# Performance work log

Hardware: AMD Instinct MI355X
Metric: run time of the kernel (lower is better)

## Reference

```python
import jax, jax.numpy as jnp
import numpy as np

XBOUND = (-30.0, 30.0, 0.25)
YBOUND = (-15.0, 15.0, 0.25)
ZBOUND = (-1.0, 1.0, 0.5)
EPS = 1e-9


def _heights():
    n = int((ZBOUND[1] - ZBOUND[0]) // ZBOUND[2]) + 1
    return [ZBOUND[0] + i * ZBOUND[2] for i in range(n)]


def _bev_planes():
    # matches construct_plane_grid: linspace endpoints included, meshgrid(y, x) 'ij'
    num_x = int((XBOUND[1] - XBOUND[0]) / XBOUND[2])
    num_y = int((YBOUND[1] - YBOUND[0]) / YBOUND[2])
    x = jnp.linspace(XBOUND[0], XBOUND[1], num_x, dtype=jnp.float32)
    y = jnp.linspace(YBOUND[0], YBOUND[1], num_y, dtype=jnp.float32)
    yy, xx = jnp.meshgrid(y, x, indexing='ij')
    planes = [jnp.stack([xx, yy, jnp.full_like(xx, h)], axis=-1) for h in _heights()]
    return jnp.stack(planes)  # (nlvl, bH, bW, 3)


def _bilinear_grid_sample(im, grid):
    # faithful port of the manual pad+floor+gather grid_sample (align_corners=False)
    n, c, h, w = im.shape
    gh, gw = grid.shape[1], grid.shape[2]
    x = ((grid[..., 0] + 1) * w - 1) / 2
    y = ((grid[..., 1] + 1) * h - 1) / 2
    x = x.reshape(n, -1)
    y = y.reshape(n, -1)
    x0 = jnp.floor(x)
    y0 = jnp.floor(y)
    wa = ((x0 + 1 - x) * (y0 + 1 - y))[:, None, :]
    wb = ((x0 + 1 - x) * (y - y0))[:, None, :]
    wc = ((x - x0) * (y0 + 1 - y))[:, None, :]
    wd = ((x - x0) * (y - y0))[:, None, :]
    pw, ph = w + 2, h + 2
    # clip in float first to avoid int32 overflow; out-of-range lands on zero padding either way
    x0f = jnp.clip(x0, -2.0, w + 2.0)
    y0f = jnp.clip(y0, -2.0, h + 2.0)
    x0i = jnp.clip(x0f.astype(jnp.int32) + 1, 0, pw - 1)
    x1i = jnp.clip(x0f.astype(jnp.int32) + 2, 0, pw - 1)
    y0i = jnp.clip(y0f.astype(jnp.int32) + 1, 0, ph - 1)
    y1i = jnp.clip(y0f.astype(jnp.int32) + 2, 0, ph - 1)
    im_flat = jnp.pad(im, ((0, 0), (0, 0), (1, 1), (1, 1))).reshape(n, c, -1)

    def gather(xi, yi):
        return jnp.take_along_axis(im_flat, (xi + yi * pw)[:, None, :], axis=2)

    out = (gather(x0i, y0i) * wa + gather(x0i, y1i) * wb
           + gather(x1i, y0i) * wc + gather(x1i, y1i) * wd)
    return out.reshape(n, c, gh, gw)


def _campos(pts, ego2cam, img_h, img_w):
    # pts: (B, q, 3); ego2cam: (B, ncam, 4, 4)
    B, q, _ = pts.shape
    ncam = ego2cam.shape[1]
    pts_h = jnp.concatenate([pts, jnp.ones_like(pts[..., :1])], axis=-1)  # (B,q,4)
    cam = jnp.einsum('bnij,bqj->bnqi', ego2cam, pts_h)  # (B,ncam,q,4)
    z = cam[..., 2:3]
    mask = z > EPS
    xy = cam[..., 0:2] / z + EPS
    px = xy[..., 0:1] / img_w
    py = xy[..., 1:2] / img_h
    p = (jnp.concatenate([px, py], axis=-1) - 0.5) * 2
    mask = (mask & (p[..., 0:1] > -1.0) & (p[..., 0:1] < 1.0)
            & (p[..., 1:2] > -1.0) & (p[..., 1:2] < 1.0))
    return p.reshape(B * ncam, q, 2), mask.reshape(B, ncam, q)


def reference(cam_feat, ego2cam, conv_w, conv_b, img_h, img_w):
    B, ncam = ego2cam.shape[0], ego2cam.shape[1]
    C = cam_feat.shape[1]
    planes = _bev_planes().astype(cam_feat.dtype)  # (nlvl,bH,bW,3)
    nlvl, bH, bW, _ = planes.shape
    pts = jnp.broadcast_to(planes.reshape(1, -1, 3), (B, nlvl * bH * bW, 3))
    pos, mask = _campos(pts, ego2cam, img_h, img_w)
    grid = pos.reshape(B * ncam, nlvl * bH, bW, 2)
    proj = _bilinear_grid_sample(cam_feat, grid).reshape(B, ncam, C, nlvl, bH, bW)
    m = mask.reshape(B, ncam, 1, nlvl, bH, bW).astype(proj.dtype)
    feat = (proj * m).sum(axis=1)            # (B,C,nlvl,bH,bW)
    num = m.sum(axis=1)                      # (B,1,nlvl,bH,bW)
    feat = feat / jnp.where(num == 0, jnp.ones_like(num), num)
    coords = jnp.broadcast_to(jnp.transpose(planes, (3, 0, 1, 2))[None], (B, 3, nlvl, bH, bW))
    feat = jnp.concatenate([feat, coords], axis=1).reshape(B, (C + 3) * nlvl, bH, bW)
    out = jax.lax.conv_general_dilated(
        feat, conv_w, window_strides=(1, 1), padding=((1, 1), (1, 1)),
        dimension_numbers=('NCHW', 'OIHW', 'NCHW'))
    return out + conv_b[None, :, None, None]


def setup_inputs() -> dict:
    key = jax.random.key(0)
    k1, k2, k3 = jax.random.split(key, 3)
    B, ncam, C = 1, 6, 128
    cH, cW = 64, 176
    nlvl = 5
    cam_feat = jax.random.normal(k1, (B * ncam, C, cH, cW), dtype=jnp.float32)
    ego2cam = jax.random.normal(k2, (B, ncam, 4, 4), dtype=jnp.float32)
    conv_w = jax.random.normal(k3, (128, (C + 3) * nlvl, 3, 3), dtype=jnp.float32) * 0.02
    conv_b = jnp.zeros((128,), dtype=jnp.float32)
    return {'cam_feat': cam_feat, 'ego2cam': ego2cam, 'conv_w': conv_w,
            'conv_b': conv_b, 'img_h': 512, 'img_w': 1408}
```

## Files before the change

### kernel.cpp

```cpp
#include <hip/hip_runtime.h>
#include <hip/hip_bf16.h>

#define BH 120
#define BW 240
#define NLVL 5
#define NCAM 6
#define CH 128
#define FH 64
#define FW 176
#define CIN 655
#define CINP 672
#define NCT 21
#define FROWS 124
#define FCOLS 242
#define NPIX (BH*BW)

typedef __hip_bfloat16 bf16;
typedef __attribute__((ext_vector_type(8))) short s16x8;
typedef __attribute__((ext_vector_type(4))) float f32x4;
typedef __attribute__((ext_vector_type(2))) float f32x2;
typedef unsigned int uint;
typedef __attribute__((ext_vector_type(4), aligned(4))) uint uint4a;

#define G_AS __attribute__((address_space(1)))
#define L_AS __attribute__((address_space(3)))

__device__ __forceinline__ float bf2f(unsigned short u) {
    union { unsigned int i; float f; } c; c.i = ((unsigned int)u) << 16; return c.f;
}
__device__ __forceinline__ uint f2bu(float x) {
    return (uint)__hip_bfloat16_raw(__float2bfloat16(x)).x;
}

__global__ __launch_bounds__(256) void transpose_kernel(
    const float* __restrict__ in, float* __restrict__ out)
{
    __shared__ float t[32][129];
    int n = blockIdx.z, h = blockIdx.y, w0 = blockIdx.x * 32;
    int wlim = min(32, FW - w0);
    int wx = threadIdx.x & 31, cg = threadIdx.x >> 5;
    if (wx < wlim) {
        #pragma unroll
        for (int k = 0; k < 16; ++k) {
            int c = cg + k * 8;
            t[wx][c] = in[((n*CH + c)*FH + h)*FW + w0 + wx];
        }
    }
    __syncthreads();
    int c2 = threadIdx.x & 127, wi = threadIdx.x >> 7;
    for (int w = wi; w < wlim; w += 2)
        out[((n*FH + h)*FW + w0 + w)*CH + c2] = t[w][c2];
}

__global__ __launch_bounds__(256) void wprep_kernel(
    const float* __restrict__ w, bf16* __restrict__ wbf)
{
    int idx = blockIdx.x * 256 + threadIdx.x;
    if (idx >= 128 * CINP) return;
    int oc = idx / CINP, cin = idx - oc * CINP;
    float v[9];
    if (cin < CIN) {
        const float* s = w + ((size_t)oc * CIN + cin) * 9;
        #pragma unroll
        for (int k = 0; k < 9; ++k) v[k] = s[k];
    } else {
        #pragma unroll
        for (int k = 0; k < 9; ++k) v[k] = 0.f;
    }
    #pragma unroll
    for (int k = 0; k < 9; ++k)
        wbf[(size_t)(k * 128 + oc) * CINP + cin] = __float2bfloat16(v[k]);
}

__global__ __launch_bounds__(128) void border_kernel(bf16* __restrict__ feat)
{
    int b = blockIdx.x;
    int row, col;
    if (b < 242)      { row = 0;   col = b; }
    else if (b < 484) { row = 121; col = b - 242; }
    else if (b < 604) { row = b - 484 + 1; col = 0; }
    else              { row = b - 604 + 1; col = 241; }
    s16x8* p = (s16x8*)(feat + ((size_t)row*FCOLS + col)*CINP);
    int t = threadIdx.x;
    if (t < 84) p[t] = (s16x8){0,0,0,0,0,0,0,0};
}

__global__ __launch_bounds__(256) void proj_kernel(
    const float* __restrict__ camt,
    const float* __restrict__ e2c,
    const int* __restrict__ pimgh, const int* __restrict__ pimgw,
    bf16* __restrict__ feat)
{
    __shared__ int   s_soff[4][32];
    __shared__ float s_w4[4][30][4];
    __shared__ int   s_val[4][32];

    const int wv = threadIdx.x >> 6;
    const int lane = threadIdx.x & 63;
    const int pix = blockIdx.x * 4 + wv;
    const int bx = pix % BW, by = pix / BW;
    float xw = (float)(-30.0 + bx * (60.0/239.0)); if (bx == BW-1) xw = 30.f;
    float yw = (float)(-15.0 + by * (30.0/119.0)); if (by == BH-1) yw = 15.f;

    const bool act = lane < 30;
    int valid = 0, ix = 0, iy = 0, cam = 0;
    float fx = 0.f, fy = 0.f;
    if (act) {
        int l = lane / 6; cam = lane - l*6;
        float h = -1.f + 0.5f * (float)l;
        const float* M = e2c + cam * 16;
        float cx = M[0]*xw + M[1]*yw + M[2]*h  + M[3];
        float cy = M[4]*xw + M[5]*yw + M[6]*h  + M[7];
        float cz = M[8]*xw + M[9]*yw + M[10]*h + M[11];
        float iw = (float)pimgw[0], ih = (float)pimgh[0];
        float px = ((cx/cz + 1e-9f)/iw - 0.5f) * 2.f;
        float py = ((cy/cz + 1e-9f)/ih - 0.5f) * 2.f;
        valid = (cz > 1e-9f) && (px > -1.f) && (px < 1.f)
                             && (py > -1.f) && (py < 1.f);
        float xs = ((px + 1.f)*(float)FW - 1.f) * 0.5f;
        float ys = ((py + 1.f)*(float)FH - 1.f) * 0.5f;
        float x0 = floorf(xs), y0 = floorf(ys);
        fx = xs - x0; fy = ys - y0;
        ix = (int)x0; iy = (int)y0;
        s_val[wv][lane] = valid;
    }
    __syncthreads();
    if (act) {
        int lbase = (lane / 6) * 6;
        int cnt = s_val[wv][lbase] + s_val[wv][lbase+1] + s_val[wv][lbase+2]
                + s_val[wv][lbase+3] + s_val[wv][lbase+4] + s_val[wv][lbase+5];
        float inv = (cnt > 0) ? (1.f / (float)cnt) : 0.f;
        float sc = valid ? inv : 0.f;
        int bx0 = min(max(ix, 0), FW-2);
        int by0 = min(max(iy, 0), FH-2);
        float gx0 = (1.f - fx) * sc, gx1 = fx * sc;
        float wx0 = 0.f, wx1 = 0.f;
        if (ix >= 0)     { if (ix == bx0) wx0 += gx0; else wx1 += gx0; }
        if (ix+1 <= FW-1){ if (ix+1 == bx0) wx0 += gx1; else wx1 += gx1; }
        float wy0 = 0.f, wy1 = 0.f;
        float gy0 = 1.f - fy, gy1 = fy;
        if (iy >= 0)     { if (iy == by0) wy0 += gy0; else wy1 += gy0; }
        if (iy+1 <= FH-1){ if (iy+1 == by0) wy0 += gy1; else wy1 += gy1; }
        s_w4[wv][lane][0] = wx0 * wy0;
        s_w4[wv][lane][1] = wx0 * wy1;
        s_w4[wv][lane][2] = wx1 * wy0;
        s_w4[wv][lane][3] = wx1 * wy1;
        s_soff[wv][lane] = valid ? ((cam*FH + by0)*FW + bx0)*CH : -1;
    }
    __syncthreads();

    const int c2 = lane * 2;
    float va[NLVL], vb[NLVL];
    #pragma unroll
    for (int l = 0; l < NLVL; ++l) { va[l] = 0.f; vb[l] = 0.f; }

    #pragma unroll
    for (int l = 0; l < NLVL; ++l) {
        #pragma unroll
        for (int cm = 0; cm < NCAM; ++cm) {
            int id = l*6 + cm;
            int so = s_soff[wv][id];
            if (so >= 0) {
                const float* bp = camt + so + c2;
                f32x2 t0 = *(const f32x2*)(bp);
                f32x2 t2 = *(const f32x2*)(bp + CH);
                f32x2 t1 = *(const f32x2*)(bp + FW*CH);
                f32x2 t3 = *(const f32x2*)(bp + FW*CH + CH);
                float w0 = s_w4[wv][id][0], w1 = s_w4[wv][id][1];
                float w2 = s_w4[wv][id][2], w3 = s_w4[wv][id][3];
                va[l] += w0*t0[0] + w1*t1[0] + w2*t2[0] + w3*t3[0];
                vb[l] += w0*t0[1] + w1*t1[1] + w2*t2[1] + w3*t3[1];
            }
        }
    }

    bf16* dpix = feat + ((size_t)(by+1)*FCOLS + (bx+1))*CINP;
    uint u0 = f2bu(va[0]) | (f2bu(va[1]) << 16);
    uint u1 = f2bu(va[2]) | (f2bu(va[3]) << 16);
    uint u2 = f2bu(va[4]) | (f2bu(vb[0]) << 16);
    uint u3 = f2bu(vb[1]) | (f2bu(vb[2]) << 16);
    uint u4 = f2bu(vb[3]) | (f2bu(vb[4]) << 16);
    char* dst = (char*)(dpix + c2*5);
    *(uint4a*)dst = (uint4a){u0, u1, u2, u3};
    *(uint*)(dst + 16) = u4;
    if (lane < 15) {
        int j = lane / 5, l = lane - j*5;
        float v = (j == 0) ? xw : (j == 1) ? yw : (-1.f + 0.5f*(float)l);
        dpix[CH*5 + lane] = __float2bfloat16(v);
    }
}

__global__ __launch_bounds__(256, 4) void conv_mfma_kernel(
    const bf16* __restrict__ feat,
    const bf16* __restrict__ wbf,
    bf16* __restrict__ part)
{
    __shared__ __align__(16) char lds[40960];
    const int tid  = threadIdx.x;
    const int wv   = tid >> 6;
    const int lane = tid & 63;
    const int t15  = tid & 15;
    const int kgl  = (tid >> 4) & 3;
    const int y0p = blockIdx.y * 8;
    const int x0p = blockIdx.x * 16;
    const int q   = blockIdx.z;
    const int ct0 = q ? (1 + 5*q) : 0;
    const int nph = (q ? 5 : 6) * 9;

    const int HB0 = 0, HB1 = 12288, WB0 = 24576, WB1 = 32768;

    f32x4 acc[8][2];
    #pragma unroll
    for (int m = 0; m < 8; ++m)
        #pragma unroll
        for (int f = 0; f < 2; ++f)
            acc[m][f] = (f32x4){0.f, 0.f, 0.f, 0.f};

    auto stageW = [&](int ct, int off, int wb) {
        #pragma unroll
        for (int jj = 0; jj < 2; ++jj) {
            int j = 2*wv + jj;
            int cch = j*64 + lane;
            int oc = cch >> 2, kgp = cch & 3;
            int kg = kgp ^ ((oc >> 1) & 3);
            const bf16* src = wbf + ((size_t)(off*128 + oc)*CINP + ct*32 + kg*8);
            __builtin_amdgcn_global_load_lds((const G_AS void*)src,
                                             (L_AS void*)(lds + wb + j*1024),
                                             16, 0, 0);
        }
    };
    auto stageH = [&](int ct, int hb) {
        #pragma unroll
        for (int kk = 0; kk < 3; ++kk) {
            int j = wv + 4*kk;
            int cch = j*64 + lane;
            int pp = cch >> 2, kgp = cch & 3;
            int kg = kgp ^ ((pp >> 1) & 3);
            int row = pp / 18;
            int col = pp - row*18;
            const bf16* src = feat + ((size_t)(y0p + row)*FCOLS + (x0p + col))*CINP
                                   + ct*32 + kg*8;
            __builtin_amdgcn_global_load_lds((const G_AS void*)src,
                                             (L_AS void*)(lds + hb + j*1024),
                                             16, 0, 0);
        }
    };

    stageH(ct0, HB0);
    stageW(ct0, 0, WB0);
    __syncthreads();

    int lct = 0, off = 0;
    for (int p = 0; p < nph; ++p) {
        if (p + 1 < nph) {
            int off1 = off + 1, lct1 = lct;
            if (off1 == 9) { off1 = 0; ++lct1; }
            stageW(ct0 + lct1, off1, ((p+1) & 1) ? WB1 : WB0);
            if (off1 == 0) stageH(ct0 + lct1, (lct1 & 1) ? HB1 : HB0);
        }
        const int wb = (p & 1) ? WB1 : WB0;
        const int hb = (lct & 1) ? HB1 : HB0;
        const int ky = off / 3, kx = off - ky*3;

        s16x8 A[8];
        #pragma unroll
        for (int m = 0; m < 8; ++m) {
            int oc = m*16 + t15;
            A[m] = *(const s16x8*)(lds + wb + oc*64 + ((kgl ^ ((oc>>1)&3)) << 4));
        }
        #pragma unroll
        for (int f = 0; f < 2; ++f) {
            int prow = (2*wv + f + ky)*18 + t15 + kx;
            s16x8 Bv = *(const s16x8*)(lds + hb + prow*64 + ((kgl ^ ((prow>>1)&3)) << 4));
            __builtin_amdgcn_s_setprio(1);
            #pragma unroll
            for (int m = 0; m < 8; ++m)
                acc[m][f] = __builtin_amdgcn_mfma_f32_16x16x32_bf16(A[m], Bv, acc[m][f], 0, 0, 0);
            __builtin_amdgcn_s_setprio(0);
        }
        __syncthreads();
        if (++off == 9) { off = 0; ++lct; }
    }

    bf16* pq = part + (size_t)q * (128*NPIX);
    const int xo = x0p + t15;
    #pragma unroll
    for (int m = 0; m < 8; ++m) {
        #pragma unroll
        for (int r = 0; r < 4; ++r) {
            int oc = m*16 + kgl*4 + r;
            #pragma unroll
            for (int f = 0; f < 2; ++f) {
                int y = y0p + 2*wv + f;
                pq[(size_t)oc*NPIX + y*BW + xo] = __float2bfloat16(acc[m][f][r]);
            }
        }
    }
}

__global__ __launch_bounds__(256) void combine_kernel(
    const bf16* __restrict__ part, const float* __restrict__ bias,
    float* __restrict__ out)
{
    int i8 = blockIdx.x * 256 + threadIdx.x;
    if (i8 >= 128*NPIX/8) return;
    int oc = i8 / (NPIX/8);
    float s[8];
    float b = bias[oc];
    #pragma unroll
    for (int k = 0; k < 8; ++k) s[k] = b;
    #pragma unroll
    for (int qq = 0; qq < 4; ++qq) {
        s16x8 v = *(const s16x8*)(part + (size_t)qq*(128*NPIX) + (size_t)i8*8);
        #pragma unroll
        for (int k = 0; k < 8; ++k) s[k] += bf2f((unsigned short)v[k]);
    }
    f32x4* o = (f32x4*)(out + (size_t)i8*8);
    o[0] = (f32x4){s[0], s[1], s[2], s[3]};
    o[1] = (f32x4){s[4], s[5], s[6], s[7]};
}

extern "C" void kernel_launch(void* const* d_in, const int* in_sizes, int n_in,
                              void* d_out, int out_size, void* d_ws, size_t ws_size,
                              hipStream_t stream)
{
    const float* cam_feat = (const float*)d_in[0];
    const float* ego2cam  = (const float*)d_in[1];
    const float* conv_w   = (const float*)d_in[2];
    const float* conv_b   = (const float*)d_in[3];
    const int*   img_h    = (const int*)d_in[4];
    const int*   img_w    = (const int*)d_in[5];
    float* out = (float*)d_out;

    float* camt = (float*)d_ws;
    bf16* feat = (bf16*)(camt + (size_t)NCAM*CH*FH*FW);
    bf16* wbf  = feat + (size_t)FROWS*FCOLS*CINP;
    bf16* part = (bf16*)d_ws;

    transpose_kernel<<<dim3(6, FH, NCAM), 256, 0, stream>>>(cam_feat, camt);
    wprep_kernel<<<(128*CINP + 255)/256, 256, 0, stream>>>(conv_w, wbf);
    border_kernel<<<724, 128, 0, stream>>>(feat);
    proj_kernel<<<NPIX/4, 256, 0, stream>>>(camt, ego2cam, img_h, img_w, feat);
    conv_mfma_kernel<<<dim3(15, 15, 4), 256, 0, stream>>>(feat, wbf, part);
    combine_kernel<<<(128*NPIX/8 + 255)/256, 256, 0, stream>>>(part, conv_b, out);
}
```

Before: 118.8 us.

## Store transposed camera features in bf16 and swizzle projection block order

The transpose kernel now writes camera features as bf16 instead of fp32, and the projection kernel gathers packed bf16 pairs and unpacks them with bit shifts. This halves the bytes written by the transpose and read by the random bilinear gathers. Projection blocks are also remapped with a stride-8 swizzle so that blocks running at the same time cover spread-out BEV pixels, which changes the gather access pattern. The partial-sum buffer moves to its own workspace region, since camt no longer occupies the start of the workspace. The cost is an extra bf16 rounding of the inputs before interpolation, on top of the bf16 already used downstream.

Result: faster. 105.2 us (-11.5%).

```diff
diff --git a/kernel.cpp b/kernel.cpp
--- a/kernel.cpp
+++ b/kernel.cpp
@@ -18,7 +18,6 @@
 typedef __hip_bfloat16 bf16;
 typedef __attribute__((ext_vector_type(8))) short s16x8;
 typedef __attribute__((ext_vector_type(4))) float f32x4;
-typedef __attribute__((ext_vector_type(2))) float f32x2;
 typedef unsigned int uint;
 typedef __attribute__((ext_vector_type(4), aligned(4))) uint uint4a;
 
@@ -31,9 +30,15 @@
 __device__ __forceinline__ uint f2bu(float x) {
     return (uint)__hip_bfloat16_raw(__float2bfloat16(x)).x;
 }
+__device__ __forceinline__ float blo(uint u) {
+    union { uint i; float f; } c; c.i = u << 16; return c.f;
+}
+__device__ __forceinline__ float bhi(uint u) {
+    union { uint i; float f; } c; c.i = u & 0xFFFF0000u; return c.f;
+}
 
 __global__ __launch_bounds__(256) void transpose_kernel(
-    const float* __restrict__ in, float* __restrict__ out)
+    const float* __restrict__ in, bf16* __restrict__ out)
 {
     __shared__ float t[32][129];
     int n = blockIdx.z, h = blockIdx.y, w0 = blockIdx.x * 32;
@@ -49,7 +54,7 @@
     __syncthreads();
     int c2 = threadIdx.x & 127, wi = threadIdx.x >> 7;
     for (int w = wi; w < wlim; w += 2)
-        out[((n*FH + h)*FW + w0 + w)*CH + c2] = t[w][c2];
+        out[((n*FH + h)*FW + w0 + w)*CH + c2] = __float2bfloat16(t[w][c2]);
 }
 
 __global__ __launch_bounds__(256) void wprep_kernel(
@@ -86,7 +91,7 @@
 }
 
 __global__ __launch_bounds__(256) void proj_kernel(
-    const float* __restrict__ camt,
+    const bf16* __restrict__ camt,
     const float* __restrict__ e2c,
     const int* __restrict__ pimgh, const int* __restrict__ pimgw,
     bf16* __restrict__ feat)
@@ -97,7 +102,9 @@
 
     const int wv = threadIdx.x >> 6;
     const int lane = threadIdx.x & 63;
-    const int pix = blockIdx.x * 4 + wv;
+    const int bid = blockIdx.x;
+    const int swz = (bid & 7) * 900 + (bid >> 3);
+    const int pix = swz * 4 + wv;
     const int bx = pix % BW, by = pix / BW;
     float xw = (float)(-30.0 + bx * (60.0/239.0)); if (bx == BW-1) xw = 30.f;
     float yw = (float)(-15.0 + by * (30.0/119.0)); if (by == BH-1) yw = 15.f;
@@ -161,15 +168,15 @@
             int id = l*6 + cm;
             int so = s_soff[wv][id];
             if (so >= 0) {
-                const float* bp = camt + so + c2;
-                f32x2 t0 = *(const f32x2*)(bp);
-                f32x2 t2 = *(const f32x2*)(bp + CH);
-                f32x2 t1 = *(const f32x2*)(bp + FW*CH);
-                f32x2 t3 = *(const f32x2*)(bp + FW*CH + CH);
+                const bf16* bp = camt + so + c2;
+                uint q0 = *(const uint*)(bp);
+                uint q2 = *(const uint*)(bp + CH);
+                uint q1 = *(const uint*)(bp + FW*CH);
+                uint q3 = *(const uint*)(bp + FW*CH + CH);
                 float w0 = s_w4[wv][id][0], w1 = s_w4[wv][id][1];
                 float w2 = s_w4[wv][id][2], w3 = s_w4[wv][id][3];
-                va[l] += w0*t0[0] + w1*t1[0] + w2*t2[0] + w3*t3[0];
-                vb[l] += w0*t0[1] + w1*t1[1] + w2*t2[1] + w3*t3[1];
+                va[l] += w0*blo(q0) + w1*blo(q1) + w2*blo(q2) + w3*blo(q3);
+                vb[l] += w0*bhi(q0) + w1*bhi(q1) + w2*bhi(q2) + w3*bhi(q3);
             }
         }
     }
@@ -332,10 +339,10 @@
     const int*   img_w    = (const int*)d_in[5];
     float* out = (float*)d_out;
 
-    float* camt = (float*)d_ws;
-    bf16* feat = (bf16*)(camt + (size_t)NCAM*CH*FH*FW);
+    bf16* camt = (bf16*)d_ws;
+    bf16* feat = camt + (size_t)NCAM*CH*FH*FW;
     bf16* wbf  = feat + (size_t)FROWS*FCOLS*CINP;
-    bf16* part = (bf16*)d_ws;
+    bf16* part = wbf  + (size_t)9*128*CINP;
 
     transpose_kernel<<<dim3(6, FH, NCAM), 256, 0, stream>>>(cam_feat, camt);
     wprep_kernel<<<(128*CINP + 255)/256, 256, 0, stream>>>(conv_w, wbf);
```
